# Kernel tuning notes

Hardware: AMD Instinct MI355X
Metric: run time of the kernel (lower is better)

## Reference

```python
import jax, jax.numpy as jnp
import numpy as np

IN_FEATURES = 4096
OUT_FEATURES = 4096
GROUP_SIZE = 128
N_GROUPS = IN_FEATURES // GROUP_SIZE
N_LEVELS = 16
SCALE = float(np.sqrt(GROUP_SIZE))


def setup_inputs() -> dict:
    key = jax.random.key(0)
    k_x, k_idx, k_cb, k_norm, k_rot = jax.random.split(key, 5)
    x = jax.random.normal(k_x, (4, 2048, IN_FEATURES), dtype=jnp.float32)
    # packed 4-bit indices: each uint8 byte holds two 4-bit codes (stored as int32 here)
    indices_packed = jax.random.randint(k_idx, (OUT_FEATURES, IN_FEATURES // 2), 0, 256, dtype=jnp.int32)
    codebook = jax.random.normal(k_cb, (N_LEVELS,), dtype=jnp.float32)
    weight_norms = jax.random.uniform(k_norm, (OUT_FEATURES, N_GROUPS), dtype=jnp.float32) + 0.5
    # per-group random orthogonal rotations (QR of gaussian), matching generate_rotation_matrix semantics
    g = jax.random.normal(k_rot, (N_GROUPS, GROUP_SIZE, GROUP_SIZE), dtype=jnp.float32)
    q, _ = jnp.linalg.qr(g)
    rotations = q.astype(jnp.float32)
    return {"x": x, "indices_packed": indices_packed, "codebook": codebook,
            "weight_norms": weight_norms, "rotations": rotations}


def _unpack_4bit(packed):
    # packed: (N, K//2) -> (N, K); even columns from low nibble, odd from high nibble
    low = packed & 0xF
    high = (packed >> 4) & 0xF
    return jnp.stack([low, high], axis=-1).reshape(packed.shape[0], -1)


def reference(x, indices_packed, codebook, weight_norms, rotations):
    B, S, K = x.shape
    xf = x.reshape(-1, K).astype(jnp.float32)            # (T, K)
    T = xf.shape[0]
    # group-wise rotation: x_rot_g = x_g @ Pi_g.T
    xg = xf.reshape(T, N_GROUPS, GROUP_SIZE)             # (T, G, g)
    x_rot = jnp.einsum('tgk,gjk->tgj', xg, rotations)    # (T, G, g)
    # dequantized codes (before norm scaling)
    idx = _unpack_4bit(indices_packed)                    # (N, K)
    W = codebook[idx].reshape(OUT_FEATURES, N_GROUPS, GROUP_SIZE)  # (N, G, g)
    # out[t,n] = sum_g (x_rot[t,g,:] . W[n,g,:]) * norms[n,g] / scale
    out = jnp.einsum('tgj,ngj,ng->tn', x_rot, W, weight_norms / SCALE)
    return out.reshape(B, S, OUT_FEATURES).astype(x.dtype)
```

## Files before the change

### kernel.cpp

```cpp
#include <hip/hip_runtime.h>

typedef __attribute__((ext_vector_type(8))) __bf16 bf16x8;
typedef __attribute__((ext_vector_type(4))) float f32x4;
typedef __attribute__((ext_vector_type(4))) int i32x4;
typedef __attribute__((ext_vector_type(8))) unsigned short ushort8;

#define T_TOKENS 8192
#define K_DIM    4096
#define N_DIM    4096
#define NGRP     32
#define GS       128

__device__ __forceinline__ unsigned short f2bf(float f) {
  unsigned u = __builtin_bit_cast(unsigned, f);
  u += 0x7fffu + ((u >> 16) & 1u);
  return (unsigned short)(u >> 16);
}

__device__ __forceinline__ f32x4 mfma16(bf16x8 a, bf16x8 b, f32x4 c) {
  return __builtin_amdgcn_mfma_f32_16x16x32_bf16(a, b, c, 0, 0, 0);
}

__device__ __forceinline__ i32x4 mfma_i8(i32x4 a, i32x4 b, i32x4 c) {
  return __builtin_amdgcn_mfma_i32_16x16x64_i8(a, b, c, 0, 0, 0);
}

__device__ __forceinline__ void gload_lds16(const void* g, void* l) {
  __builtin_amdgcn_global_load_lds(
      (const __attribute__((address_space(1))) void*)g,
      (__attribute__((address_space(3))) void*)l, 16, 0, 0);
}

__device__ __forceinline__ int clamp127(int q) {
  return q > 127 ? 127 : (q < -127 ? -127 : q);
}

__global__ __launch_bounds__(256) void k_prep(const float* __restrict__ x,
                                              signed char* __restrict__ qx,
                                              float* __restrict__ sxf,
                                              const int* __restrict__ idxp,
                                              const float* __restrict__ cb,
                                              const float* __restrict__ norms,
                                              const float* __restrict__ rot,
                                              unsigned short* __restrict__ weff,
                                              int* __restrict__ swmax) {
  __shared__ unsigned short Rt[128][136];
  __shared__ unsigned short Wq[128][136];
  __shared__ float cbl[16];
  const int tid = threadIdx.x;

  if (blockIdx.x < 2048) {
    const int wid = blockIdx.x * 4 + (tid >> 6);
    const int l = tid & 63;
    const float* xr = x + (size_t)wid * K_DIM;
    float4 v[16];
    float am = 0.f;
    #pragma unroll
    for (int i = 0; i < 16; ++i) {
      v[i] = *reinterpret_cast<const float4*>(xr + (i * 64 + l) * 4);
      am = fmaxf(am, fmaxf(fmaxf(fabsf(v[i].x), fabsf(v[i].y)),
                           fmaxf(fabsf(v[i].z), fabsf(v[i].w))));
    }
    #pragma unroll
    for (int m = 1; m < 64; m <<= 1) am = fmaxf(am, __shfl_xor(am, m, 64));
    const float inv = am > 0.f ? 127.0f / am : 0.f;
    #pragma unroll
    for (int i = 0; i < 16; ++i) {
      int q0 = clamp127(__float2int_rn(v[i].x * inv));
      int q1 = clamp127(__float2int_rn(v[i].y * inv));
      int q2 = clamp127(__float2int_rn(v[i].z * inv));
      int q3 = clamp127(__float2int_rn(v[i].w * inv));
      unsigned d = (q0 & 255) | ((q1 & 255) << 8) | ((q2 & 255) << 16) |
                   ((unsigned)(q3 & 255) << 24);
      *reinterpret_cast<unsigned*>(qx + (size_t)wid * K_DIM + (size_t)(i * 64 + l) * 4) = d;
    }
    if (l == 0) sxf[wid] = am * (1.0f / 127.0f);
    return;
  }

  const int v = blockIdx.x - 2048;
  const int nt = v & 31;
  const int g  = v >> 5;
  if (tid < 16) cbl[tid] = cb[tid];

  {
    const int j = tid >> 1, kh = (tid & 1) * 64;
    const float* rp = rot + ((size_t)g * 128 + j) * 128 + kh;
    #pragma unroll
    for (int c = 0; c < 64; c += 4) {
      float4 vv = *reinterpret_cast<const float4*>(rp + c);
      Rt[kh + c + 0][j] = f2bf(vv.x);
      Rt[kh + c + 1][j] = f2bf(vv.y);
      Rt[kh + c + 2][j] = f2bf(vv.z);
      Rt[kh + c + 3][j] = f2bf(vv.w);
    }
  }
  __syncthreads();

  {
    const int nl = tid >> 1, hf = (tid & 1);
    const int* ip = idxp + ((size_t)(nt * 128 + nl)) * (K_DIM / 2) + g * 64 + hf * 32;
    #pragma unroll
    for (int c = 0; c < 32; c += 4) {
      int4 vv = *reinterpret_cast<const int4*>(ip + c);
      int va[4] = {vv.x, vv.y, vv.z, vv.w};
      #pragma unroll
      for (int q = 0; q < 4; ++q) {
        int b = va[q] & 0xFF;
        Wq[nl][hf * 64 + (c + q) * 2 + 0] = f2bf(cbl[b & 0xF]);
        Wq[nl][hf * 64 + (c + q) * 2 + 1] = f2bf(cbl[(b >> 4) & 0xF]);
      }
    }
  }
  __syncthreads();

  const int w = tid >> 6, l = tid & 63;
  const int rl = l & 15, hi = l >> 4;
  f32x4 acc[2][8] = {};
  #pragma unroll
  for (int ks = 0; ks < 4; ++ks) {
    bf16x8 a0 = *(const bf16x8*)&Wq[w * 32 +  0 + rl][ks * 32 + hi * 8];
    bf16x8 a1 = *(const bf16x8*)&Wq[w * 32 + 16 + rl][ks * 32 + hi * 8];
    #pragma unroll
    for (int nc = 0; nc < 8; ++nc) {
      bf16x8 bfr = *(const bf16x8*)&Rt[nc * 16 + rl][ks * 32 + hi * 8];
      acc[0][nc] = mfma16(a0, bfr, acc[0][nc]);
      acc[1][nc] = mfma16(a1, bfr, acc[1][nc]);
    }
  }

  const float inv_scale = 0.088388347648318447f;
  #pragma unroll
  for (int m = 0; m < 2; ++m) {
    const int r0 = nt * 128 + w * 32 + m * 16 + hi * 4;
    float nv[4];
    #pragma unroll
    for (int r = 0; r < 4; ++r) nv[r] = norms[(size_t)(r0 + r) * NGRP + g] * inv_scale;
    float rowmax[4] = {0.f, 0.f, 0.f, 0.f};
    #pragma unroll
    for (int nc = 0; nc < 8; ++nc) {
      #pragma unroll
      for (int r = 0; r < 4; ++r) {
        float wv = acc[m][nc][r] * nv[r];
        weff[(size_t)(r0 + r) * K_DIM + g * GS + nc * 16 + rl] = f2bf(wv);
        rowmax[r] = fmaxf(rowmax[r], fabsf(wv));
      }
    }
    #pragma unroll
    for (int r = 0; r < 4; ++r) {
      #pragma unroll
      for (int msk = 1; msk < 16; msk <<= 1)
        rowmax[r] = fmaxf(rowmax[r], __shfl_xor(rowmax[r], msk, 64));
      if (rl == 0) atomicMax(&swmax[r0 + r], __float_as_int(rowmax[r]));
    }
  }
}

__global__ __launch_bounds__(256) void k_wquant(const unsigned short* __restrict__ weff,
                                                const int* __restrict__ swmax,
                                                signed char* __restrict__ qw,
                                                float* __restrict__ swf) {
  const int n = blockIdx.x, t = threadIdx.x;
  const float am = __int_as_float(swmax[n]);
  const float inv = am > 0.f ? 127.0f / am : 0.f;
  const unsigned short* wr = weff + (size_t)n * K_DIM + t * 16;
  ushort8 u0 = *(const ushort8*)wr;
  ushort8 u1 = *(const ushort8*)(wr + 8);
  unsigned d[4];
  #pragma unroll
  for (int j = 0; j < 2; ++j) {
    ushort8 u = j ? u1 : u0;
    #pragma unroll
    for (int h = 0; h < 2; ++h) {
      int q0 = clamp127(__float2int_rn(__uint_as_float((unsigned)u[h * 4 + 0] << 16) * inv));
      int q1 = clamp127(__float2int_rn(__uint_as_float((unsigned)u[h * 4 + 1] << 16) * inv));
      int q2 = clamp127(__float2int_rn(__uint_as_float((unsigned)u[h * 4 + 2] << 16) * inv));
      int q3 = clamp127(__float2int_rn(__uint_as_float((unsigned)u[h * 4 + 3] << 16) * inv));
      d[j * 2 + h] = (q0 & 255) | ((q1 & 255) << 8) | ((q2 & 255) << 16) |
                     ((unsigned)(q3 & 255) << 24);
    }
  }
  *reinterpret_cast<int4*>(qw + (size_t)n * K_DIM + t * 16) =
      make_int4((int)d[0], (int)d[1], (int)d[2], (int)d[3]);
  if (t == 0) swf[n] = am * (1.0f / 127.0f);
}

#define VMW asm volatile("s_waitcnt vmcnt(4)" ::: "memory")
#define NOW ((void)0)

#define STG(gbase, koff, ldsoff) do { \
    gload_lds16((gbase) + (size_t)(koff), &lds[(ldsoff) + dst0]); \
    gload_lds16((gbase) + (size_t)(koff) + (size_t)64 * K_DIM, \
                &lds[(ldsoff) + dst0 + 4096]); \
  } while (0)

#define PHASE(qq, PAR, TAIL, ...) { \
    if ((qq) == 0) { \
      const int bb = 32768 + (PAR) * 16384 + (wc >> 1) * 8192 + ((wc & 1) * 64 + rl) * 64; \
      _Pragma("unroll") \
      for (int n = 0; n < 4; ++n) { \
        bfr[n][0] = *(const i32x4*)&lds[bb + n * 1024 + slot0]; \
        bfr[n][1] = *(const i32x4*)&lds[bb + n * 1024 + slot1]; \
      } \
    } \
    { const int ab = (PAR) * 16384 + wr * 8192 + ((qq) * 32 + rl) * 64; \
      af00 = *(const i32x4*)&lds[ab + slot0]; \
      af01 = *(const i32x4*)&lds[ab + slot1]; \
      af10 = *(const i32x4*)&lds[ab + 1024 + slot0]; \
      af11 = *(const i32x4*)&lds[ab + 1024 + slot1]; } \
    __VA_ARGS__; \
    asm volatile("s_barrier" ::: "memory"); \
    __builtin_amdgcn_s_setprio(1); \
    _Pragma("unroll") \
    for (int n = 0; n < 4; ++n) { \
      acc[(qq)*2][n]     = mfma_i8(af01, bfr[n][1], \
                             mfma_i8(af00, bfr[n][0], acc[(qq)*2][n])); \
      acc[(qq)*2 + 1][n] = mfma_i8(af11, bfr[n][1], \
                             mfma_i8(af10, bfr[n][0], acc[(qq)*2 + 1][n])); \
    } \
    __builtin_amdgcn_s_setprio(0); \
    TAIL; \
    asm volatile("s_barrier" ::: "memory"); \
  }

__global__ __launch_bounds__(512) void k_gemm(const signed char* __restrict__ A,
                                              const signed char* __restrict__ Bw,
                                              const float* __restrict__ sxf,
                                              const float* __restrict__ swf,
                                              float* __restrict__ C) {
  __shared__ unsigned short lds[65536];
  const int tid = threadIdx.x;
  const int l = tid & 63, w = tid >> 6;
  const int wr = w >> 2, wc = w & 3;
  const int rl = l & 15, hi = l >> 4;

  const int bid = blockIdx.x;
  const int xcd = bid & 7, jj = bid >> 3;
  const int brow = ((xcd >> 1) * 8 + (jj >> 3)) * 256;
  const int bcol = ((xcd & 1) * 8 + (jj & 7)) * 256;

  const int row0 = tid >> 3;
  const int gc = ((tid & 7) ^ (row0 & 7)) * 16;
  const signed char* pa  = A  + (size_t)(brow + row0) * K_DIM + gc;
  const signed char* pa2 = pa + (size_t)128 * K_DIM;
  const signed char* pb  = Bw + (size_t)(bcol + row0) * K_DIM + gc;
  const signed char* pb2 = pb + (size_t)128 * K_DIM;
  const int dst0 = tid * 8;

  const int rb7 = rl & 7;
  const int slot0 = ((0 + hi) ^ rb7) << 3;
  const int slot1 = ((4 + hi) ^ rb7) << 3;

  i32x4 acc[8][4] = {};

  STG(pb,  0,   32768);
  STG(pb2, 0,   32768 + 8192);
  STG(pa,  0,   0);
  STG(pa2, 0,   8192);
  STG(pb,  128, 32768 + 16384);
  STG(pb2, 128, 32768 + 16384 + 8192);
  asm volatile("s_waitcnt vmcnt(4)" ::: "memory");
  asm volatile("s_barrier" ::: "memory");

  for (int it = 0; it < 16; ++it) {
    const int k0  = it * 256;
    const int kA1 = k0 + 128;
    const int kN0 = (k0 + 256) & (K_DIM - 1);
    const int kN1 = (k0 + 384) & (K_DIM - 1);
    i32x4 bfr[4][2];
    i32x4 af00, af01, af10, af11;
    PHASE(0, 0, NOW, STG(pa,  kA1, 16384))
    PHASE(1, 0, NOW, STG(pa2, kA1, 16384 + 8192))
    PHASE(2, 0, NOW, STG(pb,  kN0, 32768))
    PHASE(3, 0, VMW, STG(pb2, kN0, 32768 + 8192))
    PHASE(0, 1, NOW, STG(pa,  kN0, 0))
    PHASE(1, 1, NOW, STG(pa2, kN0, 8192))
    PHASE(2, 1, NOW, STG(pb,  kN1, 32768 + 16384))
    PHASE(3, 1, VMW, STG(pb2, kN1, 32768 + 16384 + 8192))
  }

  float swv[4];
  #pragma unroll
  for (int n = 0; n < 4; ++n) swv[n] = swf[bcol + wc * 64 + n * 16 + rl];
  #pragma unroll
  for (int m = 0; m < 8; ++m) {
    const int row = brow + wr * 128 + m * 16 + hi * 4;
    float sxr[4];
    #pragma unroll
    for (int r = 0; r < 4; ++r) sxr[r] = sxf[row + r];
    #pragma unroll
    for (int n = 0; n < 4; ++n) {
      const int col = bcol + wc * 64 + n * 16 + rl;
      #pragma unroll
      for (int r = 0; r < 4; ++r)
        C[(size_t)(row + r) * N_DIM + col] = (float)acc[m][n][r] * sxr[r] * swv[n];
    }
  }
}

extern "C" void kernel_launch(void* const* d_in, const int* in_sizes, int n_in,
                              void* d_out, int out_size, void* d_ws, size_t ws_size,
                              hipStream_t stream) {
  const float* x     = (const float*)d_in[0];
  const int*   idxp  = (const int*)d_in[1];
  const float* cb    = (const float*)d_in[2];
  const float* norms = (const float*)d_in[3];
  const float* rot   = (const float*)d_in[4];
  float* out = (float*)d_out;

  unsigned short* weff = (unsigned short*)d_ws;
  signed char* qw  = (signed char*)d_ws + 33554432;
  signed char* qx  = (signed char*)d_ws + 50331648;
  float* sxf   = (float*)((char*)d_ws + 83886080);
  int*   swmax = (int*)((char*)d_ws + 83918848);
  float* swf   = (float*)((char*)d_ws + 83935232);

  hipMemsetAsync(swmax, 0, 16384, stream);
  k_prep<<<3072, 256, 0, stream>>>(x, qx, sxf, idxp, cb, norms, rot, weff, swmax);
  k_wquant<<<4096, 256, 0, stream>>>(weff, swmax, qw, swf);
  k_gemm<<<512, 512, 0, stream>>>(qx, qw, sxf, swf, out);
}
```

Baseline: 205.9 us.

## Fuse weight quantization into prep kernel with per-row-block group loop

Replaces the grid of (n-tile, group) weight blocks plus the atomicMax/memset and the separate k_wquant kernel with 64 blocks that each own 64 output rows and loop over all 32 groups. Row maxima are reduced in registers and LDS, and the same block then quantizes its rows to int8. This removes a kernel launch, a memset and the global atomics. The cost is only 64 weight blocks doing serial work, which may leave most CUs idle on the weight path, though those blocks are scheduled first alongside the x-quant blocks.

```diff
diff --git a/kernel.cpp b/kernel.cpp
--- a/kernel.cpp
+++ b/kernel.cpp
@@ -43,14 +43,16 @@
                                               const float* __restrict__ norms,
                                               const float* __restrict__ rot,
                                               unsigned short* __restrict__ weff,
-                                              int* __restrict__ swmax) {
+                                              signed char* __restrict__ qw,
+                                              float* __restrict__ swf) {
   __shared__ unsigned short Rt[128][136];
-  __shared__ unsigned short Wq[128][136];
+  __shared__ unsigned short Wq[64][136];
   __shared__ float cbl[16];
+  __shared__ float ldsmax[2][64];
   const int tid = threadIdx.x;
 
-  if (blockIdx.x < 2048) {
-    const int wid = blockIdx.x * 4 + (tid >> 6);
+  if (blockIdx.x >= 64) {
+    const int wid = (blockIdx.x - 64) * 4 + (tid >> 6);
     const int l = tid & 63;
     const float* xr = x + (size_t)wid * K_DIM;
     float4 v[16];
@@ -78,111 +80,120 @@
     return;
   }
 
-  const int v = blockIdx.x - 2048;
-  const int nt = v & 31;
-  const int g  = v >> 5;
+  const int b = blockIdx.x;
+  const int nbase = b * 64;
   if (tid < 16) cbl[tid] = cb[tid];
 
-  {
-    const int j = tid >> 1, kh = (tid & 1) * 64;
-    const float* rp = rot + ((size_t)g * 128 + j) * 128 + kh;
-    #pragma unroll
-    for (int c = 0; c < 64; c += 4) {
-      float4 vv = *reinterpret_cast<const float4*>(rp + c);
-      Rt[kh + c + 0][j] = f2bf(vv.x);
-      Rt[kh + c + 1][j] = f2bf(vv.y);
-      Rt[kh + c + 2][j] = f2bf(vv.z);
-      Rt[kh + c + 3][j] = f2bf(vv.w);
-    }
-  }
-  __syncthreads();
-
-  {
-    const int nl = tid >> 1, hf = (tid & 1);
-    const int* ip = idxp + ((size_t)(nt * 128 + nl)) * (K_DIM / 2) + g * 64 + hf * 32;
-    #pragma unroll
-    for (int c = 0; c < 32; c += 4) {
-      int4 vv = *reinterpret_cast<const int4*>(ip + c);
-      int va[4] = {vv.x, vv.y, vv.z, vv.w};
-      #pragma unroll
-      for (int q = 0; q < 4; ++q) {
-        int b = va[q] & 0xFF;
-        Wq[nl][hf * 64 + (c + q) * 2 + 0] = f2bf(cbl[b & 0xF]);
-        Wq[nl][hf * 64 + (c + q) * 2 + 1] = f2bf(cbl[(b >> 4) & 0xF]);
-      }
-    }
-  }
-  __syncthreads();
-
   const int w = tid >> 6, l = tid & 63;
+  const int wm = w >> 1, wn = w & 1;
   const int rl = l & 15, hi = l >> 4;
-  f32x4 acc[2][8] = {};
-  #pragma unroll
-  for (int ks = 0; ks < 4; ++ks) {
-    bf16x8 a0 = *(const bf16x8*)&Wq[w * 32 +  0 + rl][ks * 32 + hi * 8];
-    bf16x8 a1 = *(const bf16x8*)&Wq[w * 32 + 16 + rl][ks * 32 + hi * 8];
-    #pragma unroll
-    for (int nc = 0; nc < 8; ++nc) {
-      bf16x8 bfr = *(const bf16x8*)&Rt[nc * 16 + rl][ks * 32 + hi * 8];
-      acc[0][nc] = mfma16(a0, bfr, acc[0][nc]);
-      acc[1][nc] = mfma16(a1, bfr, acc[1][nc]);
-    }
-  }
-
+
+  float rmax[2][4] = {{0.f, 0.f, 0.f, 0.f}, {0.f, 0.f, 0.f, 0.f}};
   const float inv_scale = 0.088388347648318447f;
+
+  for (int g = 0; g < NGRP; ++g) {
+    __syncthreads();
+    {
+      const int j = tid >> 1, kh = (tid & 1) * 64;
+      const float* rp = rot + ((size_t)g * 128 + j) * 128 + kh;
+      #pragma unroll
+      for (int c = 0; c < 64; c += 4) {
+        float4 vv = *reinterpret_cast<const float4*>(rp + c);
+        Rt[kh + c + 0][j] = f2bf(vv.x);
+        Rt[kh + c + 1][j] = f2bf(vv.y);
+        Rt[kh + c + 2][j] = f2bf(vv.z);
+        Rt[kh + c + 3][j] = f2bf(vv.w);
+      }
+    }
+    {
+      const int nl = tid >> 2, qt = tid & 3;
+      const int* ip = idxp + ((size_t)(nbase + nl)) * (K_DIM / 2) + g * 64 + qt * 16;
+      #pragma unroll
+      for (int c = 0; c < 16; c += 4) {
+        int4 vv = *reinterpret_cast<const int4*>(ip + c);
+        int va[4] = {vv.x, vv.y, vv.z, vv.w};
+        #pragma unroll
+        for (int q = 0; q < 4; ++q) {
+          int bb = va[q] & 0xFF;
+          Wq[nl][qt * 32 + (c + q) * 2 + 0] = f2bf(cbl[bb & 0xF]);
+          Wq[nl][qt * 32 + (c + q) * 2 + 1] = f2bf(cbl[(bb >> 4) & 0xF]);
+        }
+      }
+    }
+    __syncthreads();
+
+    f32x4 acc[2][4] = {};
+    #pragma unroll
+    for (int ks = 0; ks < 4; ++ks) {
+      bf16x8 a0 = *(const bf16x8*)&Wq[wm * 32 +  0 + rl][ks * 32 + hi * 8];
+      bf16x8 a1 = *(const bf16x8*)&Wq[wm * 32 + 16 + rl][ks * 32 + hi * 8];
+      #pragma unroll
+      for (int nc = 0; nc < 4; ++nc) {
+        bf16x8 bfr = *(const bf16x8*)&Rt[wn * 64 + nc * 16 + rl][ks * 32 + hi * 8];
+        acc[0][nc] = mfma16(a0, bfr, acc[0][nc]);
+        acc[1][nc] = mfma16(a1, bfr, acc[1][nc]);
+      }
+    }
+
+    #pragma unroll
+    for (int m = 0; m < 2; ++m) {
+      const int r0 = nbase + wm * 32 + m * 16 + hi * 4;
+      float nv[4];
+      #pragma unroll
+      for (int r = 0; r < 4; ++r) nv[r] = norms[(size_t)(r0 + r) * NGRP + g] * inv_scale;
+      #pragma unroll
+      for (int nc = 0; nc < 4; ++nc) {
+        #pragma unroll
+        for (int r = 0; r < 4; ++r) {
+          float wv = acc[m][nc][r] * nv[r];
+          weff[(size_t)(r0 + r) * K_DIM + g * GS + wn * 64 + nc * 16 + rl] = f2bf(wv);
+          rmax[m][r] = fmaxf(rmax[m][r], fabsf(wv));
+        }
+      }
+    }
+  }
+
   #pragma unroll
   for (int m = 0; m < 2; ++m) {
-    const int r0 = nt * 128 + w * 32 + m * 16 + hi * 4;
-    float nv[4];
-    #pragma unroll
-    for (int r = 0; r < 4; ++r) nv[r] = norms[(size_t)(r0 + r) * NGRP + g] * inv_scale;
-    float rowmax[4] = {0.f, 0.f, 0.f, 0.f};
-    #pragma unroll
-    for (int nc = 0; nc < 8; ++nc) {
-      #pragma unroll
-      for (int r = 0; r < 4; ++r) {
-        float wv = acc[m][nc][r] * nv[r];
-        weff[(size_t)(r0 + r) * K_DIM + g * GS + nc * 16 + rl] = f2bf(wv);
-        rowmax[r] = fmaxf(rowmax[r], fabsf(wv));
-      }
-    }
     #pragma unroll
     for (int r = 0; r < 4; ++r) {
-      #pragma unroll
-      for (int msk = 1; msk < 16; msk <<= 1)
-        rowmax[r] = fmaxf(rowmax[r], __shfl_xor(rowmax[r], msk, 64));
-      if (rl == 0) atomicMax(&swmax[r0 + r], __float_as_int(rowmax[r]));
-    }
-  }
-}
-
-__global__ __launch_bounds__(256) void k_wquant(const unsigned short* __restrict__ weff,
-                                                const int* __restrict__ swmax,
-                                                signed char* __restrict__ qw,
-                                                float* __restrict__ swf) {
-  const int n = blockIdx.x, t = threadIdx.x;
-  const float am = __int_as_float(swmax[n]);
-  const float inv = am > 0.f ? 127.0f / am : 0.f;
-  const unsigned short* wr = weff + (size_t)n * K_DIM + t * 16;
-  ushort8 u0 = *(const ushort8*)wr;
-  ushort8 u1 = *(const ushort8*)(wr + 8);
-  unsigned d[4];
-  #pragma unroll
-  for (int j = 0; j < 2; ++j) {
-    ushort8 u = j ? u1 : u0;
-    #pragma unroll
-    for (int h = 0; h < 2; ++h) {
-      int q0 = clamp127(__float2int_rn(__uint_as_float((unsigned)u[h * 4 + 0] << 16) * inv));
-      int q1 = clamp127(__float2int_rn(__uint_as_float((unsigned)u[h * 4 + 1] << 16) * inv));
-      int q2 = clamp127(__float2int_rn(__uint_as_float((unsigned)u[h * 4 + 2] << 16) * inv));
-      int q3 = clamp127(__float2int_rn(__uint_as_float((unsigned)u[h * 4 + 3] << 16) * inv));
-      d[j * 2 + h] = (q0 & 255) | ((q1 & 255) << 8) | ((q2 & 255) << 16) |
-                     ((unsigned)(q3 & 255) << 24);
-    }
-  }
-  *reinterpret_cast<int4*>(qw + (size_t)n * K_DIM + t * 16) =
-      make_int4((int)d[0], (int)d[1], (int)d[2], (int)d[3]);
-  if (t == 0) swf[n] = am * (1.0f / 127.0f);
+      float v = rmax[m][r];
+      #pragma unroll
+      for (int msk = 1; msk < 16; msk <<= 1) v = fmaxf(v, __shfl_xor(v, msk, 64));
+      if (rl == 0) ldsmax[wn][wm * 32 + m * 16 + hi * 4 + r] = v;
+    }
+  }
+  __syncthreads();
+
+  {
+    const int lr = tid >> 2, qt = tid & 3;
+    const int n = nbase + lr;
+    const float am = fmaxf(ldsmax[0][lr], ldsmax[1][lr]);
+    const float inv = am > 0.f ? 127.0f / am : 0.f;
+    const unsigned short* wr = weff + (size_t)n * K_DIM + qt * 1024;
+    signed char* qr = qw + (size_t)n * K_DIM + qt * 1024;
+    #pragma unroll 4
+    for (int c = 0; c < 1024; c += 16) {
+      ushort8 u0 = *(const ushort8*)(wr + c);
+      ushort8 u1 = *(const ushort8*)(wr + c + 8);
+      unsigned d[4];
+      #pragma unroll
+      for (int j = 0; j < 2; ++j) {
+        ushort8 u = j ? u1 : u0;
+        #pragma unroll
+        for (int h = 0; h < 2; ++h) {
+          int q0 = clamp127(__float2int_rn(__uint_as_float((unsigned)u[h * 4 + 0] << 16) * inv));
+          int q1 = clamp127(__float2int_rn(__uint_as_float((unsigned)u[h * 4 + 1] << 16) * inv));
+          int q2 = clamp127(__float2int_rn(__uint_as_float((unsigned)u[h * 4 + 2] << 16) * inv));
+          int q3 = clamp127(__float2int_rn(__uint_as_float((unsigned)u[h * 4 + 3] << 16) * inv));
+          d[j * 2 + h] = (q0 & 255) | ((q1 & 255) << 8) | ((q2 & 255) << 16) |
+                         ((unsigned)(q3 & 255) << 24);
+        }
+      }
+      *reinterpret_cast<int4*>(qr + c) = make_int4((int)d[0], (int)d[1], (int)d[2], (int)d[3]);
+    }
+    if (qt == 0) swf[n] = am * (1.0f / 127.0f);
+  }
 }
 
 #define VMW asm volatile("s_waitcnt vmcnt(4)" ::: "memory")
@@ -312,11 +323,8 @@
   signed char* qw  = (signed char*)d_ws + 33554432;
   signed char* qx  = (signed char*)d_ws + 50331648;
   float* sxf   = (float*)((char*)d_ws + 83886080);
-  int*   swmax = (int*)((char*)d_ws + 83918848);
   float* swf   = (float*)((char*)d_ws + 83935232);
 
-  hipMemsetAsync(swmax, 0, 16384, stream);
-  k_prep<<<3072, 256, 0, stream>>>(x, qx, sxf, idxp, cb, norms, rot, weff, swmax);
-  k_wquant<<<4096, 256, 0, stream>>>(weff, swmax, qw, swf);
+  k_prep<<<2112, 256, 0, stream>>>(x, qx, sxf, idxp, cb, norms, rot, weff, qw, swf);
   k_gemm<<<512, 512, 0, stream>>>(qx, qw, sxf, swf, out);
 }
```

After: 374.7 us. 81.9% more time.
